# Optimization experiments

Hardware: AMD Instinct MI355X
Metric: run time of the kernel (lower is better)

Reference implementation:

```python
import jax, jax.numpy as jnp
import numpy as np

EXPAND = 1
N_CHUNKS = 6
CHUNK = 4

def setup_inputs() -> dict:
    key = jax.random.key(0)
    k1, k2 = jax.random.split(key)
    B = 4_000_000
    pre = jax.random.normal(k1, (B, 25), dtype=jnp.float32)
    tar = jax.random.uniform(k2, (B, 25), dtype=jnp.float32)
    return {"pre": pre, "tar": tar}

def reference(pre, tar):
    B = pre.shape[0]
    # 6 chunks of 4: softmax over each chunk, scaled by 3*expand.
    chunks = pre[:, :N_CHUNKS * CHUNK].reshape(B, N_CHUNKS, CHUNK)
    out24 = 3.0 * EXPAND * jax.nn.softmax(chunks, axis=-1)  # [B,6,4]
    tar24 = tar[:, :N_CHUNKS * CHUNK].reshape(B, N_CHUNKS, CHUNK)
    # out[24] = relu(pre[24]) is computed in the original but never enters the
    # loss (loss uses out[0:24] only), so it is omitted.
    per_sample = jnp.mean(jnp.abs(out24 - tar24), axis=(1, 2))  # mean over 24 elems
    return jnp.sum(per_sample)
```

## Files before the change

### kernel.cpp

```cpp
#include <hip/hip_runtime.h>

#define THREADS 256
#define ROWS_PER_BLOCK 256
#define ROW 25
#define TILE_FLOATS (ROWS_PER_BLOCK * ROW)
#define TILE_VEC4 (TILE_FLOATS / 4)

__launch_bounds__(THREADS)
__global__ void loss_soft_add_kernel(const float* __restrict__ pre,
                                     const float* __restrict__ tar,
                                     float* __restrict__ out, int B) {
    __shared__ float s_pre[TILE_FLOATS];
    __shared__ float s_tar[TILE_FLOATS];
    __shared__ float s_part[THREADS / 64];

    const int tid  = threadIdx.x;
    const int row0 = blockIdx.x * ROWS_PER_BLOCK;
    const int nrows = min(ROWS_PER_BLOCK, B - row0);
    const int nfloats = nrows * ROW;

    const size_t base = (size_t)row0 * ROW;

    if (nfloats == TILE_FLOATS) {
        const float4* gp = (const float4*)(pre + base);
        const float4* gt = (const float4*)(tar + base);
        float4* sp = (float4*)s_pre;
        float4* st = (float4*)s_tar;
        #pragma unroll
        for (int k = 0; k < (TILE_VEC4 + THREADS - 1) / THREADS; ++k) {
            int idx = tid + k * THREADS;
            if (idx < TILE_VEC4) {
                sp[idx] = gp[idx];
                st[idx] = gt[idx];
            }
        }
    } else {
        for (int idx = tid; idx < nfloats; idx += THREADS) {
            s_pre[idx] = pre[base + idx];
            s_tar[idx] = tar[base + idx];
        }
    }
    __syncthreads();

    float acc = 0.0f;
    if (tid < nrows) {
        const float* rp = &s_pre[tid * ROW];
        const float* rt = &s_tar[tid * ROW];
        float total = 0.0f;
        #pragma unroll
        for (int c = 0; c < 6; ++c) {
            float x0 = rp[c * 4 + 0];
            float x1 = rp[c * 4 + 1];
            float x2 = rp[c * 4 + 2];
            float x3 = rp[c * 4 + 3];
            float m = fmaxf(fmaxf(x0, x1), fmaxf(x2, x3));
            float e0 = __expf(x0 - m);
            float e1 = __expf(x1 - m);
            float e2 = __expf(x2 - m);
            float e3 = __expf(x3 - m);
            float k = 3.0f / (e0 + e1 + e2 + e3);
            total += fabsf(e0 * k - rt[c * 4 + 0]);
            total += fabsf(e1 * k - rt[c * 4 + 1]);
            total += fabsf(e2 * k - rt[c * 4 + 2]);
            total += fabsf(e3 * k - rt[c * 4 + 3]);
        }
        acc = total * (1.0f / 24.0f);
    }

    #pragma unroll
    for (int off = 32; off > 0; off >>= 1)
        acc += __shfl_down(acc, off, 64);
    const int wid = tid >> 6, lane = tid & 63;
    if (lane == 0) s_part[wid] = acc;
    __syncthreads();
    if (tid == 0) {
        float bsum = s_part[0] + s_part[1] + s_part[2] + s_part[3];
        atomicAdd(out, bsum);
    }
}

extern "C" void kernel_launch(void* const* d_in, const int* in_sizes, int n_in,
                              void* d_out, int out_size, void* d_ws, size_t ws_size,
                              hipStream_t stream) {
    const float* pre = (const float*)d_in[0];
    const float* tar = (const float*)d_in[1];
    float* out = (float*)d_out;
    const int B = in_sizes[0] / ROW;

    hipMemsetAsync(d_out, 0, sizeof(float) * out_size, stream);

    const int blocks = (B + ROWS_PER_BLOCK - 1) / ROWS_PER_BLOCK;
    loss_soft_add_kernel<<<blocks, THREADS, 0, stream>>>(pre, tar, out, B);
}
```

Measured before the change: 798.1 us.

## Use persistent grid with register prefetch and two-pass partial-sum reduction

Replaces the one-tile-per-block grid with a fixed grid of 768 persistent blocks that loop over tiles. Each block prefetches the next tile into registers while computing the current one. Per-block partial sums are written to workspace and summed by a second single-block kernel, which removes the memset and the global atomics. The register prefetch buffers (about 14 float4 values per input) raise register pressure and may limit occupancy, and an extra kernel launch is added.

```diff
diff --git a/kernel.cpp b/kernel.cpp
--- a/kernel.cpp
+++ b/kernel.cpp
@@ -1,82 +1,112 @@
 #include <hip/hip_runtime.h>
 
 #define THREADS 256
-#define ROWS_PER_BLOCK 256
+#define ROWS_PER_TILE 256
 #define ROW 25
-#define TILE_FLOATS (ROWS_PER_BLOCK * ROW)
+#define TILE_FLOATS (ROWS_PER_TILE * ROW)
 #define TILE_VEC4 (TILE_FLOATS / 4)
+#define PF_ITERS ((TILE_VEC4 + THREADS - 1) / THREADS)
+#define NBLOCKS 768
 
-__launch_bounds__(THREADS)
-__global__ void loss_soft_add_kernel(const float* __restrict__ pre,
-                                     const float* __restrict__ tar,
-                                     float* __restrict__ out, int B) {
+__global__ __launch_bounds__(THREADS, 3)
+void loss_main_kernel(const float* __restrict__ pre, const float* __restrict__ tar,
+                      float* __restrict__ partials, int B) {
     __shared__ float s_pre[TILE_FLOATS];
     __shared__ float s_tar[TILE_FLOATS];
     __shared__ float s_part[THREADS / 64];
 
-    const int tid  = threadIdx.x;
-    const int row0 = blockIdx.x * ROWS_PER_BLOCK;
-    const int nrows = min(ROWS_PER_BLOCK, B - row0);
-    const int nfloats = nrows * ROW;
+    const int tid = threadIdx.x;
+    const int ntiles = (B + ROWS_PER_TILE - 1) / ROWS_PER_TILE;
+    const long long total_vec4 = ((long long)B * ROW) / 4;
 
-    const size_t base = (size_t)row0 * ROW;
+    const float4* gp = (const float4*)pre;
+    const float4* gt = (const float4*)tar;
 
-    if (nfloats == TILE_FLOATS) {
-        const float4* gp = (const float4*)(pre + base);
-        const float4* gt = (const float4*)(tar + base);
+    float4 pf_p[PF_ITERS], pf_t[PF_ITERS];
+    float acc = 0.0f;
+
+    int tile = blockIdx.x;
+
+    if (tile < ntiles) {
+        const long long vbase = (long long)tile * TILE_VEC4;
+        #pragma unroll
+        for (int k = 0; k < PF_ITERS; ++k) {
+            int l = tid + k * THREADS;
+            long long idx = vbase + l;
+            if (l < TILE_VEC4 && idx < total_vec4) { pf_p[k] = gp[idx]; pf_t[k] = gt[idx]; }
+        }
+    }
+
+    for (; tile < ntiles; tile += NBLOCKS) {
         float4* sp = (float4*)s_pre;
         float4* st = (float4*)s_tar;
         #pragma unroll
-        for (int k = 0; k < (TILE_VEC4 + THREADS - 1) / THREADS; ++k) {
-            int idx = tid + k * THREADS;
-            if (idx < TILE_VEC4) {
-                sp[idx] = gp[idx];
-                st[idx] = gt[idx];
+        for (int k = 0; k < PF_ITERS; ++k) {
+            int l = tid + k * THREADS;
+            if (l < TILE_VEC4) { sp[l] = pf_p[k]; st[l] = pf_t[k]; }
+        }
+        __syncthreads();
+
+        const int ntile = tile + NBLOCKS;
+        if (ntile < ntiles) {
+            const long long vbase = (long long)ntile * TILE_VEC4;
+            #pragma unroll
+            for (int k = 0; k < PF_ITERS; ++k) {
+                int l = tid + k * THREADS;
+                long long idx = vbase + l;
+                if (l < TILE_VEC4 && idx < total_vec4) { pf_p[k] = gp[idx]; pf_t[k] = gt[idx]; }
             }
         }
-    } else {
-        for (int idx = tid; idx < nfloats; idx += THREADS) {
-            s_pre[idx] = pre[base + idx];
-            s_tar[idx] = tar[base + idx];
+
+        const int row = tile * ROWS_PER_TILE + tid;
+        if (row < B) {
+            const float* rp = &s_pre[tid * ROW];
+            const float* rt = &s_tar[tid * ROW];
+            float total = 0.0f;
+            #pragma unroll
+            for (int c = 0; c < 6; ++c) {
+                float x0 = rp[c * 4 + 0];
+                float x1 = rp[c * 4 + 1];
+                float x2 = rp[c * 4 + 2];
+                float x3 = rp[c * 4 + 3];
+                float m = fmaxf(fmaxf(x0, x1), fmaxf(x2, x3));
+                float e0 = __expf(x0 - m);
+                float e1 = __expf(x1 - m);
+                float e2 = __expf(x2 - m);
+                float e3 = __expf(x3 - m);
+                float kk = 3.0f / (e0 + e1 + e2 + e3);
+                total += fabsf(e0 * kk - rt[c * 4 + 0]);
+                total += fabsf(e1 * kk - rt[c * 4 + 1]);
+                total += fabsf(e2 * kk - rt[c * 4 + 2]);
+                total += fabsf(e3 * kk - rt[c * 4 + 3]);
+            }
+            acc += total * (1.0f / 24.0f);
         }
-    }
-    __syncthreads();
-
-    float acc = 0.0f;
-    if (tid < nrows) {
-        const float* rp = &s_pre[tid * ROW];
-        const float* rt = &s_tar[tid * ROW];
-        float total = 0.0f;
-        #pragma unroll
-        for (int c = 0; c < 6; ++c) {
-            float x0 = rp[c * 4 + 0];
-            float x1 = rp[c * 4 + 1];
-            float x2 = rp[c * 4 + 2];
-            float x3 = rp[c * 4 + 3];
-            float m = fmaxf(fmaxf(x0, x1), fmaxf(x2, x3));
-            float e0 = __expf(x0 - m);
-            float e1 = __expf(x1 - m);
-            float e2 = __expf(x2 - m);
-            float e3 = __expf(x3 - m);
-            float k = 3.0f / (e0 + e1 + e2 + e3);
-            total += fabsf(e0 * k - rt[c * 4 + 0]);
-            total += fabsf(e1 * k - rt[c * 4 + 1]);
-            total += fabsf(e2 * k - rt[c * 4 + 2]);
-            total += fabsf(e3 * k - rt[c * 4 + 3]);
-        }
-        acc = total * (1.0f / 24.0f);
+        __syncthreads();
     }
 
     #pragma unroll
     for (int off = 32; off > 0; off >>= 1)
         acc += __shfl_down(acc, off, 64);
-    const int wid = tid >> 6, lane = tid & 63;
-    if (lane == 0) s_part[wid] = acc;
+    if ((tid & 63) == 0) s_part[tid >> 6] = acc;
     __syncthreads();
-    if (tid == 0) {
-        float bsum = s_part[0] + s_part[1] + s_part[2] + s_part[3];
-        atomicAdd(out, bsum);
-    }
+    if (tid == 0)
+        partials[blockIdx.x] = s_part[0] + s_part[1] + s_part[2] + s_part[3];
+}
+
+__global__ __launch_bounds__(THREADS)
+void loss_reduce_kernel(const float* __restrict__ partials, float* __restrict__ out, int n) {
+    __shared__ float s_part[THREADS / 64];
+    const int tid = threadIdx.x;
+    float v = 0.0f;
+    for (int i = tid; i < n; i += THREADS) v += partials[i];
+    #pragma unroll
+    for (int off = 32; off > 0; off >>= 1)
+        v += __shfl_down(v, off, 64);
+    if ((tid & 63) == 0) s_part[tid >> 6] = v;
+    __syncthreads();
+    if (tid == 0)
+        out[0] = s_part[0] + s_part[1] + s_part[2] + s_part[3];
 }
 
 extern "C" void kernel_launch(void* const* d_in, const int* in_sizes, int n_in,
@@ -85,10 +115,9 @@
     const float* pre = (const float*)d_in[0];
     const float* tar = (const float*)d_in[1];
     float* out = (float*)d_out;
+    float* partials = (float*)d_ws;
     const int B = in_sizes[0] / ROW;
 
-    hipMemsetAsync(d_out, 0, sizeof(float) * out_size, stream);
-
-    const int blocks = (B + ROWS_PER_BLOCK - 1) / ROWS_PER_BLOCK;
-    loss_soft_add_kernel<<<blocks, THREADS, 0, stream>>>(pre, tar, out, B);
+    loss_main_kernel<<<NBLOCKS, THREADS, 0, stream>>>(pre, tar, partials, B);
+    loss_reduce_kernel<<<1, THREADS, 0, stream>>>(partials, out, NBLOCKS);
 }
```

Result: slower. 904.0 us (+13.3%).
